# Optimization experiments

Hardware: AMD Instinct MI355X
Metric: run time of the kernel (lower is better)

## Reference

```python
import jax, jax.numpy as jnp
import numpy as np

HID = 128
SCALE = np.sqrt(HID)


def _ln(x, g, b, eps=1e-5):
    m = jnp.mean(x, axis=-1, keepdims=True)
    v = jnp.mean((x - m) ** 2, axis=-1, keepdims=True)
    return (x - m) * jax.lax.rsqrt(v + eps) * g + b


def _attention(img, txt, Wi, bi, Wt, bt, g1, b1, Wq, bq, Wk, bk, Wv, bv, g2, b2, Wo, bo):
    # img: [..., S, image_dim], txt: [..., S, text_dim] -> [..., S, HID]
    c = img @ Wi.T + bi + txt @ Wt.T + bt
    c = _ln(c, g1, b1)
    q = c @ Wq.T + bq
    k = c @ Wk.T + bk
    v = c @ Wv.T + bv
    s = jnp.einsum('...qd,...kd->...qk', q, k) / (SCALE + 1e-8)
    a = jax.nn.softmax(s, axis=-1)
    a = a + 1e-10
    a = a / jnp.sum(a, axis=-1, keepdims=True)
    a = jnp.clip(a, 1e-7, 1.0)
    ctx = jnp.einsum('...qk,...kd->...qd', a, v)
    ctx = _ln(ctx, g2, b2)
    return ctx @ Wo.T + bo


def setup_inputs() -> dict:
    key = jax.random.key(0)
    ks = jax.random.split(key, 24)
    T, Q, DI, DT = 256, 64, 2048, 768

    def xavier(k, shape):
        fan_in, fan_out = shape[1], shape[0]
        lim = np.sqrt(6.0 / (fan_in + fan_out))
        return jax.random.uniform(k, shape, jnp.float32, -lim, lim)

    return {
        'support_images': jax.random.normal(ks[0], (T, 4, DI), jnp.float32),
        'support_texts': jax.random.normal(ks[1], (T, 4, DT), jnp.float32),
        'support_labels': jax.random.randint(ks[2], (T, 4), 0, 4, jnp.int64),
        'query_images': jax.random.normal(ks[3], (T, Q, DI), jnp.float32),
        'query_texts': jax.random.normal(ks[4], (T, Q, DT), jnp.float32),
        'Wi': xavier(ks[5], (HID, DI)), 'bi': jnp.zeros((HID,)),
        'Wt': xavier(ks[6], (HID, DT)), 'bt': jnp.zeros((HID,)),
        'g1': jnp.ones((HID,)), 'b1': jnp.zeros((HID,)),
        'Wq': xavier(ks[7], (HID, HID)), 'bq': jnp.zeros((HID,)),
        'Wk': xavier(ks[8], (HID, HID)), 'bk': jnp.zeros((HID,)),
        'Wv': xavier(ks[9], (HID, HID)), 'bv': jnp.zeros((HID,)),
        'g2': jnp.ones((HID,)), 'b2': jnp.zeros((HID,)),
        'Wo': xavier(ks[10], (HID, HID)), 'bo': jnp.zeros((HID,)),
    }


def reference(support_images, support_texts, support_labels, query_images, query_texts,
              Wi, bi, Wt, bt, g1, b1, Wq, bq, Wk, bk, Wv, bv, g2, b2, Wo, bo):
    p = (Wi, bi, Wt, bt, g1, b1, Wq, bq, Wk, bk, Wv, bv, g2, b2, Wo, bo)
    # Support: attention across the 4 support items of each task -> [T, 4, HID]
    support_feats = _attention(support_images, support_texts, *p)
    # Queries: source processes each query alone (seq len 1) -> add singleton seq axis
    qf = _attention(query_images[:, :, None, :], query_texts[:, :, None, :], *p)
    qf = qf[:, :, 0, :]  # [T, Q, HID]
    # Cosine-similarity prototype scoring (eps=1e-8 as in F.cosine_similarity)
    qn = qf / jnp.clip(jnp.linalg.norm(qf, axis=-1, keepdims=True), 1e-8, None)
    pn = support_feats / jnp.clip(jnp.linalg.norm(support_feats, axis=-1, keepdims=True), 1e-8, None)
    logits = jnp.einsum('tqd,tcd->tqc', qn, pn) * 10.0  # [T, Q, 4]
    return logits
```

## Files before the change

### kernel.cpp

```cpp
#include <hip/hip_runtime.h>

typedef __bf16 bf16_t;
typedef __attribute__((ext_vector_type(4))) __bf16 bf16x4;
typedef __attribute__((ext_vector_type(8))) __bf16 bf16x8;
typedef __attribute__((ext_vector_type(4))) float floatx4;

#define LN_EPS 1e-5f

__device__ __forceinline__ void dma16(const void* g, void* l) {
    __builtin_amdgcn_global_load_lds(
        (const __attribute__((address_space(1))) void*)g,
        (__attribute__((address_space(3))) void*)l, 16, 0, 0);
}

__global__ __launch_bounds__(256) void k0_prep(
    const float* __restrict__ bi, const float* __restrict__ bt,
    const float* __restrict__ Wq, const float* __restrict__ Wk,
    const float* __restrict__ Wv, const float* __restrict__ Wo,
    float* __restrict__ c_all, bf16_t* __restrict__ wbf)
{
    const int b = blockIdx.x;
    if (b < 2176) {
        int i = b * 256 + threadIdx.x;
        int c4 = i & 31;
        float4 a = ((const float4*)bi)[c4];
        float4 bb = ((const float4*)bt)[c4];
        float4 v; v.x = a.x + bb.x; v.y = a.y + bb.y; v.z = a.z + bb.z; v.w = a.w + bb.w;
        ((float4*)c_all)[i] = v;
    } else {
        int i4 = (b - 2176) * 256 + threadIdx.x;
        int which = i4 >> 12;
        int off4  = i4 & 4095;
        const float* W = (which == 0) ? Wq : (which == 1) ? Wk : (which == 2) ? Wv : Wo;
        float4 v = ((const float4*)W)[off4];
        bf16x4 pk; pk.x = (bf16_t)v.x; pk.y = (bf16_t)v.y;
                   pk.z = (bf16_t)v.z; pk.w = (bf16_t)v.w;
        *(bf16x4*)&wbf[which * 16384 + off4 * 4] = pk;
    }
}

__global__ __launch_bounds__(256, 4) void k1_gemm(
    const float* __restrict__ qimg, const float* __restrict__ qtxt,
    const float* __restrict__ simg, const float* __restrict__ stxt,
    const float* __restrict__ Wi,   const float* __restrict__ Wt,
    float* __restrict__ c_all)
{
    __shared__ float lA[64 * 32];
    __shared__ float lB[128 * 32];

    const int tid  = threadIdx.x;
    const int m0   = blockIdx.x * 64;
    const int chnk = blockIdx.y;
    const bool isq = (m0 < 16384);
    const int rb   = isq ? m0 : (m0 - 16384);
    const float* Aimg = isq ? qimg : simg;
    const float* Atxt = isq ? qtxt : stxt;

    const int wid  = tid >> 6;
    const int lane = tid & 63;
    const int quad = lane >> 4;
    const int l16  = lane & 15;
    const int wr   = wid >> 1;
    const int wc   = wid & 1;

    const int jr = lane >> 3;
    const int cA = (lane & 7) ^ jr;

    floatx4 acc[2][4];
#pragma unroll
    for (int i = 0; i < 2; ++i)
#pragma unroll
        for (int j = 0; j < 4; ++j) acc[i][j] = (floatx4)0.f;

    for (int s = 0; s < 22; ++s) {
        const int k0 = chnk * 704 + s * 32;
        const float* abase; const float* bbase; size_t lda, ldb;
        if (k0 < 2048) {
            abase = Aimg + (size_t)rb * 2048 + k0; lda = 2048;
            bbase = Wi + k0;                        ldb = 2048;
        } else {
            abase = Atxt + (size_t)rb * 768 + (k0 - 2048); lda = 768;
            bbase = Wt + (k0 - 2048);                       ldb = 768;
        }
        __syncthreads();
#pragma unroll
        for (int ii = 0; ii < 2; ++ii) {
            int i = 2 * wid + ii;
            dma16(abase + (size_t)(8 * i + jr) * lda + (cA << 2),
                  (char*)lA + i * 1024);
        }
#pragma unroll
        for (int ii = 0; ii < 4; ++ii) {
            int i = 4 * wid + ii;
            dma16(bbase + (size_t)(8 * i + jr) * ldb + (cA << 2),
                  (char*)lB + i * 1024);
        }
        __syncthreads();

        const int x7 = l16 & 7;
        bf16x8 af[2], bfr[4];
#pragma unroll
        for (int mt = 0; mt < 2; ++mt) {
            int R = wr * 32 + mt * 16 + l16;
            float4 f0 = *(const float4*)&lA[R * 32 + (((2 * quad)     ^ x7) << 2)];
            float4 f1 = *(const float4*)&lA[R * 32 + (((2 * quad + 1) ^ x7) << 2)];
            bf16x8 a;
            a[0] = (bf16_t)f0.x; a[1] = (bf16_t)f0.y; a[2] = (bf16_t)f0.z; a[3] = (bf16_t)f0.w;
            a[4] = (bf16_t)f1.x; a[5] = (bf16_t)f1.y; a[6] = (bf16_t)f1.z; a[7] = (bf16_t)f1.w;
            af[mt] = a;
        }
#pragma unroll
        for (int nt = 0; nt < 4; ++nt) {
            int R = wc * 64 + nt * 16 + l16;
            float4 f0 = *(const float4*)&lB[R * 32 + (((2 * quad)     ^ x7) << 2)];
            float4 f1 = *(const float4*)&lB[R * 32 + (((2 * quad + 1) ^ x7) << 2)];
            bf16x8 b;
            b[0] = (bf16_t)f0.x; b[1] = (bf16_t)f0.y; b[2] = (bf16_t)f0.z; b[3] = (bf16_t)f0.w;
            b[4] = (bf16_t)f1.x; b[5] = (bf16_t)f1.y; b[6] = (bf16_t)f1.z; b[7] = (bf16_t)f1.w;
            bfr[nt] = b;
        }
#pragma unroll
        for (int mt = 0; mt < 2; ++mt)
#pragma unroll
            for (int nt = 0; nt < 4; ++nt)
                acc[mt][nt] = __builtin_amdgcn_mfma_f32_16x16x32_bf16(
                    af[mt], bfr[nt], acc[mt][nt], 0, 0, 0);
    }
#pragma unroll
    for (int nt = 0; nt < 4; ++nt) {
        int col = wc * 64 + nt * 16 + l16;
#pragma unroll
        for (int mt = 0; mt < 2; ++mt)
#pragma unroll
            for (int r = 0; r < 4; ++r) {
                int row = wr * 32 + mt * 16 + quad * 4 + r;
                unsafeAtomicAdd(&c_all[(size_t)(m0 + row) * 128 + col], acc[mt][nt][r]);
            }
    }
}

#define K2_ST 136

__global__ __launch_bounds__(256) void k2_query(
    const float* __restrict__ c_all, const bf16_t* __restrict__ wbf,
    const float* __restrict__ bv, const float* __restrict__ bo,
    const float* __restrict__ g1, const float* __restrict__ b1,
    const float* __restrict__ g2, const float* __restrict__ b2,
    const float* __restrict__ pn, float* __restrict__ out)
{
    __shared__ bf16_t tT[64 * K2_ST];
    __shared__ bf16_t tW[128 * 128];
    __shared__ float  pl[4][132];

    const int tid  = threadIdx.x;
    const int wid  = tid >> 6;
    const int lane = tid & 63;
    const int quad = lane >> 4;
    const int l16  = lane & 15;
    const int task = blockIdx.x;
    const int t0   = task * 64;
    const int r0   = wid * 16;

    const bf16_t* Wvb = wbf + 2 * 16384;
    const bf16_t* Wob = wbf + 3 * 16384;

    const int jr4 = lane >> 4;
    const int jp  = lane & 15;
#pragma unroll
    for (int ii = 0; ii < 8; ++ii) {
        int i = 8 * wid + ii;
        int row = 4 * i + jr4;
        int c = jp ^ (row & 15);
        dma16(Wvb + row * 128 + c * 8, (char*)tW + i * 1024);
    }
    if (tid < 128) {
        int r = tid >> 5, c4 = tid & 31;
        *(float4*)&pl[r][c4 * 4] = *(const float4*)(pn + ((size_t)task * 4 + r) * 128 + c4 * 4);
    }

    float bvr[8], g2r[8], b2r[8], bor[8];
#pragma unroll
    for (int nt = 0; nt < 8; ++nt) {
        int col = nt * 16 + l16;
        bvr[nt] = bv[col]; g2r[nt] = g2[col]; b2r[nt] = b2[col]; bor[nt] = bo[col];
    }

    const int g8 = lane >> 3;
    const int s8 = lane & 7;
    float g1a[16], b1a[16];
#pragma unroll
    for (int mm = 0; mm < 4; ++mm) {
        *(float4*)&g1a[mm * 4] = ((const float4*)(g1 + s8 * 16))[mm];
        *(float4*)&b1a[mm * 4] = ((const float4*)(b1 + s8 * 16))[mm];
    }
#pragma unroll
    for (int p = 0; p < 2; ++p) {
        int rloc = r0 + p * 8 + g8;
        const float* src = c_all + (size_t)(t0 + rloc) * 128 + s8 * 16;
        float v[16];
#pragma unroll
        for (int mm = 0; mm < 4; ++mm) *(float4*)&v[mm * 4] = ((const float4*)src)[mm];
        float s = 0.f, q = 0.f;
#pragma unroll
        for (int m = 0; m < 16; ++m) { s += v[m]; q += v[m] * v[m]; }
#pragma unroll
        for (int m = 1; m < 8; m <<= 1) { s += __shfl_xor(s, m); q += __shfl_xor(q, m); }
        float mean = s * (1.f / 128.f);
        float var  = q * (1.f / 128.f) - mean * mean;
        float rs   = rsqrtf(var + LN_EPS);
        bf16x8 o0, o1;
#pragma unroll
        for (int m = 0; m < 8; ++m)  o0[m] = (bf16_t)((v[m] - mean) * rs * g1a[m] + b1a[m]);
#pragma unroll
        for (int m = 0; m < 8; ++m)  o1[m] = (bf16_t)((v[8 + m] - mean) * rs * g1a[8 + m] + b1a[8 + m]);
        *(bf16x8*)&tT[rloc * K2_ST + s8 * 16]     = o0;
        *(bf16x8*)&tT[rloc * K2_ST + s8 * 16 + 8] = o1;
    }
    __syncthreads();

    floatx4 acc[8];
#pragma unroll
    for (int nt = 0; nt < 8; ++nt) acc[nt] = (floatx4)0.f;
#pragma unroll
    for (int ks = 0; ks < 4; ++ks) {
        bf16x8 a = *(const bf16x8*)&tT[(r0 + l16) * K2_ST + ks * 32 + quad * 8];
#pragma unroll
        for (int nt = 0; nt < 8; ++nt) {
            bf16x8 b = *(const bf16x8*)&tW[(nt * 16 + l16) * 128 + (((ks * 4 + quad) ^ l16) << 3)];
            acc[nt] = __builtin_amdgcn_mfma_f32_16x16x32_bf16(a, b, acc[nt], 0, 0, 0);
        }
    }
#pragma unroll
    for (int nt = 0; nt < 8; ++nt)
#pragma unroll
        for (int r = 0; r < 4; ++r) acc[nt][r] += bvr[nt];

#pragma unroll
    for (int r = 0; r < 4; ++r) {
        float s = 0.f, q = 0.f;
#pragma unroll
        for (int nt = 0; nt < 8; ++nt) { float x = acc[nt][r]; s += x; q += x * x; }
#pragma unroll
        for (int m = 1; m < 16; m <<= 1) { s += __shfl_xor(s, m); q += __shfl_xor(q, m); }
        float mean = s * (1.f / 128.f);
        float var  = q * (1.f / 128.f) - mean * mean;
        float rs   = rsqrtf(var + LN_EPS);
        int row = r0 + quad * 4 + r;
#pragma unroll
        for (int nt = 0; nt < 8; ++nt)
            tT[row * K2_ST + nt * 16 + l16] = (bf16_t)((acc[nt][r] - mean) * rs * g2r[nt] + b2r[nt]);
    }
    __syncthreads();
#pragma unroll
    for (int ii = 0; ii < 8; ++ii) {
        int i = 8 * wid + ii;
        int row = 4 * i + jr4;
        int c = jp ^ (row & 15);
        dma16(Wob + row * 128 + c * 8, (char*)tW + i * 1024);
    }
    __syncthreads();

#pragma unroll
    for (int nt = 0; nt < 8; ++nt) acc[nt] = (floatx4)0.f;
#pragma unroll
    for (int ks = 0; ks < 4; ++ks) {
        bf16x8 a = *(const bf16x8*)&tT[(r0 + l16) * K2_ST + ks * 32 + quad * 8];
#pragma unroll
        for (int nt = 0; nt < 8; ++nt) {
            bf16x8 b = *(const bf16x8*)&tW[(nt * 16 + l16) * 128 + (((ks * 4 + quad) ^ l16) << 3)];
            acc[nt] = __builtin_amdgcn_mfma_f32_16x16x32_bf16(a, b, acc[nt], 0, 0, 0);
        }
    }

#pragma unroll
    for (int r = 0; r < 4; ++r) {
        float st[8]; float q = 0.f;
#pragma unroll
        for (int nt = 0; nt < 8; ++nt) {
            float x = acc[nt][r] + bor[nt]; st[nt] = x; q += x * x;
        }
#pragma unroll
        for (int m = 1; m < 16; m <<= 1) q += __shfl_xor(q, m);
        float inv = 1.f / fmaxf(sqrtf(q), 1e-8f);
        float d0 = 0.f, d1 = 0.f, d2 = 0.f, d3 = 0.f;
#pragma unroll
        for (int nt = 0; nt < 8; ++nt) {
            float xn = st[nt] * inv;
            int col = nt * 16 + l16;
            d0 += xn * pl[0][col]; d1 += xn * pl[1][col];
            d2 += xn * pl[2][col]; d3 += xn * pl[3][col];
        }
#pragma unroll
        for (int m = 1; m < 16; m <<= 1) {
            d0 += __shfl_xor(d0, m); d1 += __shfl_xor(d1, m);
            d2 += __shfl_xor(d2, m); d3 += __shfl_xor(d3, m);
        }
        if (l16 == 0) {
            int qi = r0 + quad * 4 + r;
            float* o = out + (size_t)task * 256 + qi * 4;
            o[0] = d0 * 10.f; o[1] = d1 * 10.f; o[2] = d2 * 10.f; o[3] = d3 * 10.f;
        }
    }
}

__global__ __launch_bounds__(256) void k3_support(
    const float* __restrict__ c_all, const bf16_t* __restrict__ wbf,
    const float* __restrict__ bq, const float* __restrict__ bk,
    const float* __restrict__ bv, const float* __restrict__ bo,
    const float* __restrict__ g1, const float* __restrict__ b1,
    const float* __restrict__ g2, const float* __restrict__ b2,
    float* __restrict__ pn)
{
    __shared__ float  cs[4][128];
    __shared__ bf16_t tW[128 * 128];
    __shared__ float  qkv[3][4][128];
    __shared__ float  att[4][4];
    __shared__ float  ctx[4][128];

    const int tid  = threadIdx.x;
    const int wid  = tid >> 6;
    const int lane = tid & 63;
    const int task = blockIdx.x;
    const int jr4  = lane >> 4;
    const int jp   = lane & 15;

    {
        const float* src = c_all + (size_t)(16384 + task * 4 + wid) * 128;
        float x0 = src[lane], x1 = src[64 + lane];
        float s = x0 + x1, q = x0 * x0 + x1 * x1;
#pragma unroll
        for (int m = 1; m < 64; m <<= 1) { s += __shfl_xor(s, m); q += __shfl_xor(q, m); }
        float mean = s * (1.f / 128.f);
        float var  = q * (1.f / 128.f) - mean * mean;
        float rs   = rsqrtf(var + LN_EPS);
        cs[wid][lane]      = (x0 - mean) * rs * g1[lane] + b1[lane];
        cs[wid][64 + lane] = (x1 - mean) * rs * g1[64 + lane] + b1[64 + lane];
    }

    const float* Bs[3] = { bq, bk, bv };
    for (int w = 0; w < 3; ++w) {
        __syncthreads();
#pragma unroll
        for (int ii = 0; ii < 8; ++ii) {
            int i = 8 * wid + ii;
            int row = 4 * i + jr4;
            int c = jp ^ (row & 15);
            dma16(wbf + w * 16384 + row * 128 + c * 8, (char*)tW + i * 1024);
        }
        __syncthreads();
#pragma unroll
        for (int j = 0; j < 2; ++j) {
            int o = tid + j * 256;
            int s = o >> 7, n = o & 127;
            const float4* c4 = (const float4*)cs[s];
            float acc = 0.f;
#pragma unroll
            for (int c = 0; c < 16; ++c) {
                bf16x8 wv = *(const bf16x8*)&tW[n * 128 + ((c ^ (n & 15)) << 3)];
                float4 a0 = c4[c * 2], a1 = c4[c * 2 + 1];
                acc += a0.x * (float)wv[0] + a0.y * (float)wv[1]
                     + a0.z * (float)wv[2] + a0.w * (float)wv[3]
                     + a1.x * (float)wv[4] + a1.y * (float)wv[5]
                     + a1.z * (float)wv[6] + a1.w * (float)wv[7];
            }
            qkv[w][s][n] = acc + Bs[w][n];
        }
    }
    __syncthreads();
    if (tid < 16) {
        int i = tid >> 2, j = tid & 3;
        const float4* qv = (const float4*)qkv[0][i];
        const float4* kv = (const float4*)qkv[1][j];
        float acc = 0.f;
#pragma unroll
        for (int k = 0; k < 32; ++k) {
            float4 a = qv[k], b = kv[k];
            acc += a.x * b.x + a.y * b.y + a.z * b.z + a.w * b.w;
        }
        att[i][j] = acc * (float)(1.0 / (11.313708498984761 + 1e-8));
    }
    __syncthreads();
    if (tid < 4) {
        float s0 = att[tid][0], s1 = att[tid][1], s2 = att[tid][2], s3 = att[tid][3];
        float m = fmaxf(fmaxf(s0, s1), fmaxf(s2, s3));
        float e0 = expf(s0 - m), e1 = expf(s1 - m), e2 = expf(s2 - m), e3 = expf(s3 - m);
        float se = e0 + e1 + e2 + e3;
        float a0 = e0 / se + 1e-10f, a1 = e1 / se + 1e-10f;
        float a2 = e2 / se + 1e-10f, a3 = e3 / se + 1e-10f;
        float t = a0 + a1 + a2 + a3;
        att[tid][0] = fminf(fmaxf(a0 / t, 1e-7f), 1.f);
        att[tid][1] = fminf(fmaxf(a1 / t, 1e-7f), 1.f);
        att[tid][2] = fminf(fmaxf(a2 / t, 1e-7f), 1.f);
        att[tid][3] = fminf(fmaxf(a3 / t, 1e-7f), 1.f);
    }
    __syncthreads();
#pragma unroll
    for (int j = 0; j < 2; ++j) {
        int o = tid + j * 256;
        int s = o >> 7, n = o & 127;
        ctx[s][n] = att[s][0] * qkv[2][0][n] + att[s][1] * qkv[2][1][n]
                  + att[s][2] * qkv[2][2][n] + att[s][3] * qkv[2][3][n];
    }
    __syncthreads();
    {
        float x0 = ctx[wid][lane], x1 = ctx[wid][64 + lane];
        float s = x0 + x1, q = x0 * x0 + x1 * x1;
#pragma unroll
        for (int m = 1; m < 64; m <<= 1) { s += __shfl_xor(s, m); q += __shfl_xor(q, m); }
        float mean = s * (1.f / 128.f);
        float var  = q * (1.f / 128.f) - mean * mean;
        float rs   = rsqrtf(var + LN_EPS);
        cs[wid][lane]      = (x0 - mean) * rs * g2[lane] + b2[lane];
        cs[wid][64 + lane] = (x1 - mean) * rs * g2[64 + lane] + b2[64 + lane];
    }
    __syncthreads();
#pragma unroll
    for (int ii = 0; ii < 8; ++ii) {
        int i = 8 * wid + ii;
        int row = 4 * i + jr4;
        int c = jp ^ (row & 15);
        dma16(wbf + 3 * 16384 + row * 128 + c * 8, (char*)tW + i * 1024);
    }
    __syncthreads();
#pragma unroll
    for (int j = 0; j < 2; ++j) {
        int o = tid + j * 256;
        int s = o >> 7, n = o & 127;
        const float4* c4 = (const float4*)cs[s];
        float acc = 0.f;
#pragma unroll
        for (int c = 0; c < 16; ++c) {
            bf16x8 wv = *(const bf16x8*)&tW[n * 128 + ((c ^ (n & 15)) << 3)];
            float4 a0 = c4[c * 2], a1 = c4[c * 2 + 1];
            acc += a0.x * (float)wv[0] + a0.y * (float)wv[1]
                 + a0.z * (float)wv[2] + a0.w * (float)wv[3]
                 + a1.x * (float)wv[4] + a1.y * (float)wv[5]
                 + a1.z * (float)wv[6] + a1.w * (float)wv[7];
        }
        ctx[s][n] = acc + bo[n];
    }
    __syncthreads();
    {
        float x0 = ctx[wid][lane], x1 = ctx[wid][64 + lane];
        float q = x0 * x0 + x1 * x1;
#pragma unroll
        for (int m = 1; m < 64; m <<= 1) q += __shfl_xor(q, m);
        float inv = 1.f / fmaxf(sqrtf(q), 1e-8f);
        float* dst = pn + (size_t)(task * 4 + wid) * 128;
        dst[lane]      = x0 * inv;
        dst[64 + lane] = x1 * inv;
    }
}

extern "C" void kernel_launch(void* const* d_in, const int* in_sizes, int n_in,
                              void* d_out, int out_size, void* d_ws, size_t ws_size,
                              hipStream_t stream)
{
    const float* simg = (const float*)d_in[0];
    const float* stxt = (const float*)d_in[1];
    const float* qimg = (const float*)d_in[3];
    const float* qtxt = (const float*)d_in[4];
    const float* Wi = (const float*)d_in[5];
    const float* bi = (const float*)d_in[6];
    const float* Wt = (const float*)d_in[7];
    const float* bt = (const float*)d_in[8];
    const float* g1 = (const float*)d_in[9];
    const float* b1 = (const float*)d_in[10];
    const float* Wq = (const float*)d_in[11];
    const float* bq = (const float*)d_in[12];
    const float* Wk = (const float*)d_in[13];
    const float* bk = (const float*)d_in[14];
    const float* Wv = (const float*)d_in[15];
    const float* bv = (const float*)d_in[16];
    const float* g2 = (const float*)d_in[17];
    const float* b2 = (const float*)d_in[18];
    const float* Wo = (const float*)d_in[19];
    const float* bo = (const float*)d_in[20];
    float* out = (float*)d_out;

    float*  c_all = (float*)d_ws;
    float*  pn    = c_all + (size_t)17408 * 128;
    bf16_t* wbf   = (bf16_t*)(pn + (size_t)1024 * 128);

    k0_prep<<<2240, 256, 0, stream>>>(bi, bt, Wq, Wk, Wv, Wo, c_all, wbf);
    k1_gemm<<<dim3(272, 4), 256, 0, stream>>>(qimg, qtxt, simg, stxt, Wi, Wt, c_all);
    k3_support<<<256, 256, 0, stream>>>(c_all, wbf, bq, bk, bv, bo, g1, b1, g2, b2, pn);
    k2_query<<<256, 256, 0, stream>>>(c_all, wbf, bv, bo, g1, b1, g2, b2, pn, out);
}
```

Measured before the change: 325.6 us.

## Pre-convert Wi/Wt to bf16, load GEMM operands directly, fuse support and query kernels

The prep kernel now also converts Wi and Wt to bf16. The big projection GEMM drops its LDS staging and barriers and loads fp32 activations and bf16 weights straight from global memory into MFMA fragments. This halves weight traffic and removes the per-step syncthreads, but each wave now issues uncoalesced 32-byte row-strided loads with no reuse through shared memory. The support-attention and query kernels are merged into one launch that keeps the prototypes in LDS, which removes a launch and the pn round-trip through global memory.

```diff
diff --git a/kernel.cpp b/kernel.cpp
--- a/kernel.cpp
+++ b/kernel.cpp
@@ -13,10 +13,14 @@
         (__attribute__((address_space(3))) void*)l, 16, 0, 0);
 }
 
+#define WBF_WI 65536
+#define WBF_WT (65536 + 262144)
+
 __global__ __launch_bounds__(256) void k0_prep(
     const float* __restrict__ bi, const float* __restrict__ bt,
     const float* __restrict__ Wq, const float* __restrict__ Wk,
     const float* __restrict__ Wv, const float* __restrict__ Wo,
+    const float* __restrict__ Wi, const float* __restrict__ Wt,
     float* __restrict__ c_all, bf16_t* __restrict__ wbf)
 {
     const int b = blockIdx.x;
@@ -29,24 +33,64 @@
         ((float4*)c_all)[i] = v;
     } else {
         int i4 = (b - 2176) * 256 + threadIdx.x;
-        int which = i4 >> 12;
-        int off4  = i4 & 4095;
-        const float* W = (which == 0) ? Wq : (which == 1) ? Wk : (which == 2) ? Wv : Wo;
-        float4 v = ((const float4*)W)[off4];
+        const float* src; int dst;
+        if (i4 < 16384) {
+            int which = i4 >> 12, off4 = i4 & 4095;
+            src = ((which == 0) ? Wq : (which == 1) ? Wk : (which == 2) ? Wv : Wo) + off4 * 4;
+            dst = which * 16384 + off4 * 4;
+        } else if (i4 < 16384 + 65536) {
+            int off4 = i4 - 16384;
+            src = Wi + off4 * 4; dst = WBF_WI + off4 * 4;
+        } else {
+            int off4 = i4 - (16384 + 65536);
+            src = Wt + off4 * 4; dst = WBF_WT + off4 * 4;
+        }
+        float4 v = *(const float4*)src;
         bf16x4 pk; pk.x = (bf16_t)v.x; pk.y = (bf16_t)v.y;
                    pk.z = (bf16_t)v.z; pk.w = (bf16_t)v.w;
-        *(bf16x4*)&wbf[which * 16384 + off4 * 4] = pk;
+        *(bf16x4*)&wbf[dst] = pk;
     }
 }
+
+#define K1_MFMA8(FA0, FA1)                                                     \
+    acc[0][0] = __builtin_amdgcn_mfma_f32_16x16x32_bf16(FA0, fb0, acc[0][0], 0, 0, 0); \
+    acc[0][1] = __builtin_amdgcn_mfma_f32_16x16x32_bf16(FA0, fb1, acc[0][1], 0, 0, 0); \
+    acc[0][2] = __builtin_amdgcn_mfma_f32_16x16x32_bf16(FA0, fb2, acc[0][2], 0, 0, 0); \
+    acc[0][3] = __builtin_amdgcn_mfma_f32_16x16x32_bf16(FA0, fb3, acc[0][3], 0, 0, 0); \
+    acc[1][0] = __builtin_amdgcn_mfma_f32_16x16x32_bf16(FA1, fb0, acc[1][0], 0, 0, 0); \
+    acc[1][1] = __builtin_amdgcn_mfma_f32_16x16x32_bf16(FA1, fb1, acc[1][1], 0, 0, 0); \
+    acc[1][2] = __builtin_amdgcn_mfma_f32_16x16x32_bf16(FA1, fb2, acc[1][2], 0, 0, 0); \
+    acc[1][3] = __builtin_amdgcn_mfma_f32_16x16x32_bf16(FA1, fb3, acc[1][3], 0, 0, 0);
+
+#define K1_BODY(A0, A1, B0, B1, B2, B3, K)                                     \
+    {                                                                          \
+        float4 p00 = *(const float4*)((A0) + (K));                             \
+        float4 p01 = *(const float4*)((A0) + (K) + 4);                         \
+        float4 p10 = *(const float4*)((A1) + (K));                             \
+        float4 p11 = *(const float4*)((A1) + (K) + 4);                         \
+        bf16x8 fb0 = *(const bf16x8*)((B0) + (K));                             \
+        bf16x8 fb1 = *(const bf16x8*)((B1) + (K));                             \
+        bf16x8 fb2 = *(const bf16x8*)((B2) + (K));                             \
+        bf16x8 fb3 = *(const bf16x8*)((B3) + (K));                             \
+        bf16x8 fa0, fa1;                                                       \
+        fa0[0] = (bf16_t)p00.x; fa0[1] = (bf16_t)p00.y;                        \
+        fa0[2] = (bf16_t)p00.z; fa0[3] = (bf16_t)p00.w;                        \
+        fa0[4] = (bf16_t)p01.x; fa0[5] = (bf16_t)p01.y;                        \
+        fa0[6] = (bf16_t)p01.z; fa0[7] = (bf16_t)p01.w;                        \
+        fa1[0] = (bf16_t)p10.x; fa1[1] = (bf16_t)p10.y;                        \
+        fa1[2] = (bf16_t)p10.z; fa1[3] = (bf16_t)p10.w;                        \
+        fa1[4] = (bf16_t)p11.x; fa1[5] = (bf16_t)p11.y;                        \
+        fa1[6] = (bf16_t)p11.z; fa1[7] = (bf16_t)p11.w;                        \
+        K1_MFMA8(fa0, fa1)                                                     \
+    }
 
 __global__ __launch_bounds__(256, 4) void k1_gemm(
     const float* __restrict__ qimg, const float* __restrict__ qtxt,
     const float* __restrict__ simg, const float* __restrict__ stxt,
-    const float* __restrict__ Wi,   const float* __restrict__ Wt,
-    float* __restrict__ c_all)
+    const bf16_t* __restrict__ wbf, float* __restrict__ c_all)
 {
-    __shared__ float lA[64 * 32];
-    __shared__ float lB[128 * 32];
+    const bf16_t* Wib = wbf + WBF_WI;
+    const bf16_t* Wtb = wbf + WBF_WT;
 
     const int tid  = threadIdx.x;
     const int m0   = blockIdx.x * 64;
@@ -63,8 +107,8 @@
     const int wr   = wid >> 1;
     const int wc   = wid & 1;
 
-    const int jr = lane >> 3;
-    const int cA = (lane & 7) ^ jr;
+    const int ar0 = rb + wr * 32 + l16;
+    const int bc0 = wc * 64 + l16;
 
     floatx4 acc[2][4];
 #pragma unroll
@@ -72,60 +116,35 @@
 #pragma unroll
         for (int j = 0; j < 4; ++j) acc[i][j] = (floatx4)0.f;
 
-    for (int s = 0; s < 22; ++s) {
-        const int k0 = chnk * 704 + s * 32;
-        const float* abase; const float* bbase; size_t lda, ldb;
-        if (k0 < 2048) {
-            abase = Aimg + (size_t)rb * 2048 + k0; lda = 2048;
-            bbase = Wi + k0;                        ldb = 2048;
-        } else {
-            abase = Atxt + (size_t)rb * 768 + (k0 - 2048); lda = 768;
-            bbase = Wt + (k0 - 2048);                       ldb = 768;
-        }
-        __syncthreads();
-#pragma unroll
-        for (int ii = 0; ii < 2; ++ii) {
-            int i = 2 * wid + ii;
-            dma16(abase + (size_t)(8 * i + jr) * lda + (cA << 2),
-                  (char*)lA + i * 1024);
-        }
-#pragma unroll
-        for (int ii = 0; ii < 4; ++ii) {
-            int i = 4 * wid + ii;
-            dma16(bbase + (size_t)(8 * i + jr) * ldb + (cA << 2),
-                  (char*)lB + i * 1024);
-        }
-        __syncthreads();
-
-        const int x7 = l16 & 7;
-        bf16x8 af[2], bfr[4];
-#pragma unroll
-        for (int mt = 0; mt < 2; ++mt) {
-            int R = wr * 32 + mt * 16 + l16;
-            float4 f0 = *(const float4*)&lA[R * 32 + (((2 * quad)     ^ x7) << 2)];
-            float4 f1 = *(const float4*)&lA[R * 32 + (((2 * quad + 1) ^ x7) << 2)];
-            bf16x8 a;
-            a[0] = (bf16_t)f0.x; a[1] = (bf16_t)f0.y; a[2] = (bf16_t)f0.z; a[3] = (bf16_t)f0.w;
-            a[4] = (bf16_t)f1.x; a[5] = (bf16_t)f1.y; a[6] = (bf16_t)f1.z; a[7] = (bf16_t)f1.w;
-            af[mt] = a;
-        }
-#pragma unroll
-        for (int nt = 0; nt < 4; ++nt) {
-            int R = wc * 64 + nt * 16 + l16;
-            float4 f0 = *(const float4*)&lB[R * 32 + (((2 * quad)     ^ x7) << 2)];
-            float4 f1 = *(const float4*)&lB[R * 32 + (((2 * quad + 1) ^ x7) << 2)];
-            bf16x8 b;
-            b[0] = (bf16_t)f0.x; b[1] = (bf16_t)f0.y; b[2] = (bf16_t)f0.z; b[3] = (bf16_t)f0.w;
-            b[4] = (bf16_t)f1.x; b[5] = (bf16_t)f1.y; b[6] = (bf16_t)f1.z; b[7] = (bf16_t)f1.w;
-            bfr[nt] = b;
-        }
-#pragma unroll
-        for (int mt = 0; mt < 2; ++mt)
-#pragma unroll
-            for (int nt = 0; nt < 4; ++nt)
-                acc[mt][nt] = __builtin_amdgcn_mfma_f32_16x16x32_bf16(
-                    af[mt], bfr[nt], acc[mt][nt], 0, 0, 0);
-    }
+    const int kb = chnk * 704;
+    const int ke = kb + 704;
+
+    const int ie = (ke < 2048) ? ke : 2048;
+    if (kb < ie) {
+        const float*  a0 = Aimg + (size_t)ar0 * 2048 + quad * 8 + kb;
+        const float*  a1 = a0 + (size_t)16 * 2048;
+        const bf16_t* b0 = Wib + (size_t)bc0 * 2048 + quad * 8 + kb;
+        const bf16_t* b1 = b0 + (size_t)16 * 2048;
+        const bf16_t* b2 = b0 + (size_t)32 * 2048;
+        const bf16_t* b3 = b0 + (size_t)48 * 2048;
+        const int n = ie - kb;
+#pragma unroll 2
+        for (int k = 0; k < n; k += 32) K1_BODY(a0, a1, b0, b1, b2, b3, k)
+    }
+    const int ts = (kb > 2048) ? kb : 2048;
+    if (ts < ke) {
+        const int off = ts - 2048;
+        const float*  a0 = Atxt + (size_t)ar0 * 768 + quad * 8 + off;
+        const float*  a1 = a0 + (size_t)16 * 768;
+        const bf16_t* b0 = Wtb + (size_t)bc0 * 768 + quad * 8 + off;
+        const bf16_t* b1 = b0 + (size_t)16 * 768;
+        const bf16_t* b2 = b0 + (size_t)32 * 768;
+        const bf16_t* b3 = b0 + (size_t)48 * 768;
+        const int n = ke - ts;
+#pragma unroll 2
+        for (int k = 0; k < n; k += 32) K1_BODY(a0, a1, b0, b1, b2, b3, k)
+    }
+
 #pragma unroll
     for (int nt = 0; nt < 4; ++nt) {
         int col = wc * 64 + nt * 16 + l16;
@@ -141,15 +160,19 @@
 
 #define K2_ST 136
 
-__global__ __launch_bounds__(256) void k2_query(
+__global__ __launch_bounds__(256) void k2_fused(
     const float* __restrict__ c_all, const bf16_t* __restrict__ wbf,
+    const float* __restrict__ bq, const float* __restrict__ bk,
     const float* __restrict__ bv, const float* __restrict__ bo,
     const float* __restrict__ g1, const float* __restrict__ b1,
     const float* __restrict__ g2, const float* __restrict__ b2,
-    const float* __restrict__ pn, float* __restrict__ out)
+    float* __restrict__ out)
 {
     __shared__ bf16_t tT[64 * K2_ST];
     __shared__ bf16_t tW[128 * 128];
+    __shared__ float  cs[4][128];
+    __shared__ float  qkv[3][4][128];
+    __shared__ float  att[4][4];
     __shared__ float  pl[4][132];
 
     const int tid  = threadIdx.x;
@@ -160,22 +183,15 @@
     const int task = blockIdx.x;
     const int t0   = task * 64;
     const int r0   = wid * 16;
-
-    const bf16_t* Wvb = wbf + 2 * 16384;
-    const bf16_t* Wob = wbf + 3 * 16384;
-
-    const int jr4 = lane >> 4;
-    const int jp  = lane & 15;
+    const int jr4  = lane >> 4;
+    const int jp   = lane & 15;
+
 #pragma unroll
     for (int ii = 0; ii < 8; ++ii) {
         int i = 8 * wid + ii;
         int row = 4 * i + jr4;
         int c = jp ^ (row & 15);
-        dma16(Wvb + row * 128 + c * 8, (char*)tW + i * 1024);
-    }
-    if (tid < 128) {
-        int r = tid >> 5, c4 = tid & 31;
-        *(float4*)&pl[r][c4 * 4] = *(const float4*)(pn + ((size_t)task * 4 + r) * 128 + c4 * 4);
+        dma16(wbf + 0 * 16384 + row * 128 + c * 8, (char*)tW + i * 1024);
     }
 
     float bvr[8], g2r[8], b2r[8], bor[8];
@@ -185,145 +201,38 @@
         bvr[nt] = bv[col]; g2r[nt] = g2[col]; b2r[nt] = b2[col]; bor[nt] = bo[col];
     }
 
-    const int g8 = lane >> 3;
-    const int s8 = lane & 7;
-    float g1a[16], b1a[16];
-#pragma unroll
-    for (int mm = 0; mm < 4; ++mm) {
-        *(float4*)&g1a[mm * 4] = ((const float4*)(g1 + s8 * 16))[mm];
-        *(float4*)&b1a[mm * 4] = ((const float4*)(b1 + s8 * 16))[mm];
-    }
-#pragma unroll
-    for (int p = 0; p < 2; ++p) {
-        int rloc = r0 + p * 8 + g8;
-        const float* src = c_all + (size_t)(t0 + rloc) * 128 + s8 * 16;
-        float v[16];
-#pragma unroll
-        for (int mm = 0; mm < 4; ++mm) *(float4*)&v[mm * 4] = ((const float4*)src)[mm];
-        float s = 0.f, q = 0.f;
-#pragma unroll
-        for (int m = 0; m < 16; ++m) { s += v[m]; q += v[m] * v[m]; }
-#pragma unroll
-        for (int m = 1; m < 8; m <<= 1) { s += __shfl_xor(s, m); q += __shfl_xor(q, m); }
-        float mean = s * (1.f / 128.f);
-        float var  = q * (1.f / 128.f) - mean * mean;
-        float rs   = rsqrtf(var + LN_EPS);
-        bf16x8 o0, o1;
-#pragma unroll
-        for (int m = 0; m < 8; ++m)  o0[m] = (bf16_t)((v[m] - mean) * rs * g1a[m] + b1a[m]);
-#pragma unroll
-        for (int m = 0; m < 8; ++m)  o1[m] = (bf16_t)((v[8 + m] - mean) * rs * g1a[8 + m] + b1a[8 + m]);
-        *(bf16x8*)&tT[rloc * K2_ST + s8 * 16]     = o0;
-        *(bf16x8*)&tT[rloc * K2_ST + s8 * 16 + 8] = o1;
-    }
-    __syncthreads();
-
-    floatx4 acc[8];
-#pragma unroll
-    for (int nt = 0; nt < 8; ++nt) acc[nt] = (floatx4)0.f;
-#pragma unroll
-    for (int ks = 0; ks < 4; ++ks) {
-        bf16x8 a = *(const bf16x8*)&tT[(r0 + l16) * K2_ST + ks * 32 + quad * 8];
-#pragma unroll
-        for (int nt = 0; nt < 8; ++nt) {
-            bf16x8 b = *(const bf16x8*)&tW[(nt * 16 + l16) * 128 + (((ks * 4 + quad) ^ l16) << 3)];
-            acc[nt] = __builtin_amdgcn_mfma_f32_16x16x32_bf16(a, b, acc[nt], 0, 0, 0);
-        }
-    }
-#pragma unroll
-    for (int nt = 0; nt < 8; ++nt)
-#pragma unroll
-        for (int r = 0; r < 4; ++r) acc[nt][r] += bvr[nt];
-
-#pragma unroll
-    for (int r = 0; r < 4; ++r) {
-        float s = 0.f, q = 0.f;
-#pragma unroll
-        for (int nt = 0; nt < 8; ++nt) { float x = acc[nt][r]; s += x; q += x * x; }
-#pragma unroll
-        for (int m = 1; m < 16; m <<= 1) { s += __shfl_xor(s, m); q += __shfl_xor(q, m); }
-        float mean = s * (1.f / 128.f);
-        float var  = q * (1.f / 128.f) - mean * mean;
-        float rs   = rsqrtf(var + LN_EPS);
-        int row = r0 + quad * 4 + r;
-#pragma unroll
-        for (int nt = 0; nt < 8; ++nt)
-            tT[row * K2_ST + nt * 16 + l16] = (bf16_t)((acc[nt][r] - mean) * rs * g2r[nt] + b2r[nt]);
-    }
-    __syncthreads();
-#pragma unroll
-    for (int ii = 0; ii < 8; ++ii) {
-        int i = 8 * wid + ii;
-        int row = 4 * i + jr4;
-        int c = jp ^ (row & 15);
-        dma16(Wob + row * 128 + c * 8, (char*)tW + i * 1024);
-    }
-    __syncthreads();
-
-#pragma unroll
-    for (int nt = 0; nt < 8; ++nt) acc[nt] = (floatx4)0.f;
-#pragma unroll
-    for (int ks = 0; ks < 4; ++ks) {
-        bf16x8 a = *(const bf16x8*)&tT[(r0 + l16) * K2_ST + ks * 32 + quad * 8];
-#pragma unroll
-        for (int nt = 0; nt < 8; ++nt) {
-            bf16x8 b = *(const bf16x8*)&tW[(nt * 16 + l16) * 128 + (((ks * 4 + quad) ^ l16) << 3)];
-            acc[nt] = __builtin_amdgcn_mfma_f32_16x16x32_bf16(a, b, acc[nt], 0, 0, 0);
-        }
-    }
-
-#pragma unroll
-    for (int r = 0; r < 4; ++r) {
-        float st[8]; float q = 0.f;
-#pragma unroll
-        for (int nt = 0; nt < 8; ++nt) {
-            float x = acc[nt][r] + bor[nt]; st[nt] = x; q += x * x;
-        }
-#pragma unroll
-        for (int m = 1; m < 16; m <<= 1) q += __shfl_xor(q, m);
-        float inv = 1.f / fmaxf(sqrtf(q), 1e-8f);
-        float d0 = 0.f, d1 = 0.f, d2 = 0.f, d3 = 0.f;
-#pragma unroll
-        for (int nt = 0; nt < 8; ++nt) {
-            float xn = st[nt] * inv;
-            int col = nt * 16 + l16;
-            d0 += xn * pl[0][col]; d1 += xn * pl[1][col];
-            d2 += xn * pl[2][col]; d3 += xn * pl[3][col];
-        }
-#pragma unroll
-        for (int m = 1; m < 16; m <<= 1) {
-            d0 += __shfl_xor(d0, m); d1 += __shfl_xor(d1, m);
-            d2 += __shfl_xor(d2, m); d3 += __shfl_xor(d3, m);
-        }
-        if (l16 == 0) {
-            int qi = r0 + quad * 4 + r;
-            float* o = out + (size_t)task * 256 + qi * 4;
-            o[0] = d0 * 10.f; o[1] = d1 * 10.f; o[2] = d2 * 10.f; o[3] = d3 * 10.f;
-        }
-    }
-}
-
-__global__ __launch_bounds__(256) void k3_support(
-    const float* __restrict__ c_all, const bf16_t* __restrict__ wbf,
-    const float* __restrict__ bq, const float* __restrict__ bk,
-    const float* __restrict__ bv, const float* __restrict__ bo,
-    const float* __restrict__ g1, const float* __restrict__ b1,
-    const float* __restrict__ g2, const float* __restrict__ b2,
-    float* __restrict__ pn)
-{
-    __shared__ float  cs[4][128];
-    __shared__ bf16_t tW[128 * 128];
-    __shared__ float  qkv[3][4][128];
-    __shared__ float  att[4][4];
-    __shared__ float  ctx[4][128];
-
-    const int tid  = threadIdx.x;
-    const int wid  = tid >> 6;
-    const int lane = tid & 63;
-    const int task = blockIdx.x;
-    const int jr4  = lane >> 4;
-    const int jp   = lane & 15;
-
+    {
+        const int g8 = lane >> 3, s8 = lane & 7;
+        float g1a[16], b1a[16];
+#pragma unroll
+        for (int mm = 0; mm < 4; ++mm) {
+            *(float4*)&g1a[mm * 4] = ((const float4*)(g1 + s8 * 16))[mm];
+            *(float4*)&b1a[mm * 4] = ((const float4*)(b1 + s8 * 16))[mm];
+        }
+#pragma unroll
+        for (int p = 0; p < 2; ++p) {
+            int rloc = r0 + p * 8 + g8;
+            const float* src = c_all + (size_t)(t0 + rloc) * 128 + s8 * 16;
+            float v[16];
+#pragma unroll
+            for (int mm = 0; mm < 4; ++mm) *(float4*)&v[mm * 4] = ((const float4*)src)[mm];
+            float s = 0.f, q = 0.f;
+#pragma unroll
+            for (int m = 0; m < 16; ++m) { s += v[m]; q += v[m] * v[m]; }
+#pragma unroll
+            for (int m = 1; m < 8; m <<= 1) { s += __shfl_xor(s, m); q += __shfl_xor(q, m); }
+            float mean = s * (1.f / 128.f);
+            float var  = q * (1.f / 128.f) - mean * mean;
+            float rs   = rsqrtf(var + LN_EPS);
+            bf16x8 o0, o1;
+#pragma unroll
+            for (int m = 0; m < 8; ++m) o0[m] = (bf16_t)((v[m] - mean) * rs * g1a[m] + b1a[m]);
+#pragma unroll
+            for (int m = 0; m < 8; ++m) o1[m] = (bf16_t)((v[8 + m] - mean) * rs * g1a[8 + m] + b1a[8 + m]);
+            *(bf16x8*)&tT[rloc * K2_ST + s8 * 16]     = o0;
+            *(bf16x8*)&tT[rloc * K2_ST + s8 * 16 + 8] = o1;
+        }
+    }
     {
         const float* src = c_all + (size_t)(16384 + task * 4 + wid) * 128;
         float x0 = src[lane], x1 = src[64 + lane];
@@ -336,50 +245,127 @@
         cs[wid][lane]      = (x0 - mean) * rs * g1[lane] + b1[lane];
         cs[wid][64 + lane] = (x1 - mean) * rs * g1[64 + lane] + b1[64 + lane];
     }
-
-    const float* Bs[3] = { bq, bk, bv };
-    for (int w = 0; w < 3; ++w) {
-        __syncthreads();
-#pragma unroll
-        for (int ii = 0; ii < 8; ++ii) {
-            int i = 8 * wid + ii;
-            int row = 4 * i + jr4;
-            int c = jp ^ (row & 15);
-            dma16(wbf + w * 16384 + row * 128 + c * 8, (char*)tW + i * 1024);
-        }
-        __syncthreads();
-#pragma unroll
-        for (int j = 0; j < 2; ++j) {
-            int o = tid + j * 256;
-            int s = o >> 7, n = o & 127;
-            const float4* c4 = (const float4*)cs[s];
-            float acc = 0.f;
-#pragma unroll
-            for (int c = 0; c < 16; ++c) {
-                bf16x8 wv = *(const bf16x8*)&tW[n * 128 + ((c ^ (n & 15)) << 3)];
-                float4 a0 = c4[c * 2], a1 = c4[c * 2 + 1];
-                acc += a0.x * (float)wv[0] + a0.y * (float)wv[1]
-                     + a0.z * (float)wv[2] + a0.w * (float)wv[3]
-                     + a1.x * (float)wv[4] + a1.y * (float)wv[5]
-                     + a1.z * (float)wv[6] + a1.w * (float)wv[7];
-            }
-            qkv[w][s][n] = acc + Bs[w][n];
-        }
-    }
-    __syncthreads();
+    __syncthreads();
+
+#pragma unroll
+    for (int j = 0; j < 2; ++j) {
+        int o = tid + j * 256, s = o >> 7, n = o & 127;
+        const float4* c4 = (const float4*)cs[s];
+        float acc = 0.f;
+#pragma unroll
+        for (int c = 0; c < 16; ++c) {
+            bf16x8 wv = *(const bf16x8*)&tW[n * 128 + ((c ^ (n & 15)) << 3)];
+            float4 a0 = c4[c * 2], a1 = c4[c * 2 + 1];
+            acc += a0.x * (float)wv[0] + a0.y * (float)wv[1]
+                 + a0.z * (float)wv[2] + a0.w * (float)wv[3]
+                 + a1.x * (float)wv[4] + a1.y * (float)wv[5]
+                 + a1.z * (float)wv[6] + a1.w * (float)wv[7];
+        }
+        qkv[0][s][n] = acc + bq[n];
+    }
+    __syncthreads();
+#pragma unroll
+    for (int ii = 0; ii < 8; ++ii) {
+        int i = 8 * wid + ii;
+        int row = 4 * i + jr4;
+        int c = jp ^ (row & 15);
+        dma16(wbf + 1 * 16384 + row * 128 + c * 8, (char*)tW + i * 1024);
+    }
+    __syncthreads();
+#pragma unroll
+    for (int j = 0; j < 2; ++j) {
+        int o = tid + j * 256, s = o >> 7, n = o & 127;
+        const float4* c4 = (const float4*)cs[s];
+        float acc = 0.f;
+#pragma unroll
+        for (int c = 0; c < 16; ++c) {
+            bf16x8 wv = *(const bf16x8*)&tW[n * 128 + ((c ^ (n & 15)) << 3)];
+            float4 a0 = c4[c * 2], a1 = c4[c * 2 + 1];
+            acc += a0.x * (float)wv[0] + a0.y * (float)wv[1]
+                 + a0.z * (float)wv[2] + a0.w * (float)wv[3]
+                 + a1.x * (float)wv[4] + a1.y * (float)wv[5]
+                 + a1.z * (float)wv[6] + a1.w * (float)wv[7];
+        }
+        qkv[1][s][n] = acc + bk[n];
+    }
+    __syncthreads();
+#pragma unroll
+    for (int ii = 0; ii < 8; ++ii) {
+        int i = 8 * wid + ii;
+        int row = 4 * i + jr4;
+        int c = jp ^ (row & 15);
+        dma16(wbf + 2 * 16384 + row * 128 + c * 8, (char*)tW + i * 1024);
+    }
+    __syncthreads();
+
+    floatx4 acc[8];
+#pragma unroll
+    for (int nt = 0; nt < 8; ++nt) acc[nt] = (floatx4)0.f;
+#pragma unroll
+    for (int ks = 0; ks < 4; ++ks) {
+        bf16x8 a = *(const bf16x8*)&tT[(r0 + l16) * K2_ST + ks * 32 + quad * 8];
+#pragma unroll
+        for (int nt = 0; nt < 8; ++nt) {
+            bf16x8 b = *(const bf16x8*)&tW[(nt * 16 + l16) * 128 + (((ks * 4 + quad) ^ l16) << 3)];
+            acc[nt] = __builtin_amdgcn_mfma_f32_16x16x32_bf16(a, b, acc[nt], 0, 0, 0);
+        }
+    }
+#pragma unroll
+    for (int nt = 0; nt < 8; ++nt)
+#pragma unroll
+        for (int r = 0; r < 4; ++r) acc[nt][r] += bvr[nt];
+
+#pragma unroll
+    for (int j = 0; j < 2; ++j) {
+        int o = tid + j * 256, s = o >> 7, n = o & 127;
+        const float4* c4 = (const float4*)cs[s];
+        float a = 0.f;
+#pragma unroll
+        for (int c = 0; c < 16; ++c) {
+            bf16x8 wv = *(const bf16x8*)&tW[n * 128 + ((c ^ (n & 15)) << 3)];
+            float4 a0 = c4[c * 2], a1 = c4[c * 2 + 1];
+            a += a0.x * (float)wv[0] + a0.y * (float)wv[1]
+               + a0.z * (float)wv[2] + a0.w * (float)wv[3]
+               + a1.x * (float)wv[4] + a1.y * (float)wv[5]
+               + a1.z * (float)wv[6] + a1.w * (float)wv[7];
+        }
+        qkv[2][s][n] = a + bv[n];
+    }
     if (tid < 16) {
         int i = tid >> 2, j = tid & 3;
         const float4* qv = (const float4*)qkv[0][i];
         const float4* kv = (const float4*)qkv[1][j];
-        float acc = 0.f;
+        float a = 0.f;
 #pragma unroll
         for (int k = 0; k < 32; ++k) {
-            float4 a = qv[k], b = kv[k];
-            acc += a.x * b.x + a.y * b.y + a.z * b.z + a.w * b.w;
-        }
-        att[i][j] = acc * (float)(1.0 / (11.313708498984761 + 1e-8));
-    }
-    __syncthreads();
+            float4 x = qv[k], y = kv[k];
+            a += x.x * y.x + x.y * y.y + x.z * y.z + x.w * y.w;
+        }
+        att[i][j] = a * (float)(1.0 / (11.313708498984761 + 1e-8));
+    }
+#pragma unroll
+    for (int r = 0; r < 4; ++r) {
+        float s = 0.f, q = 0.f;
+#pragma unroll
+        for (int nt = 0; nt < 8; ++nt) { float x = acc[nt][r]; s += x; q += x * x; }
+#pragma unroll
+        for (int m = 1; m < 16; m <<= 1) { s += __shfl_xor(s, m); q += __shfl_xor(q, m); }
+        float mean = s * (1.f / 128.f);
+        float var  = q * (1.f / 128.f) - mean * mean;
+        float rs   = rsqrtf(var + LN_EPS);
+        int row = r0 + quad * 4 + r;
+#pragma unroll
+        for (int nt = 0; nt < 8; ++nt)
+            tT[row * K2_ST + nt * 16 + l16] = (bf16_t)((acc[nt][r] - mean) * rs * g2r[nt] + b2r[nt]);
+    }
+    __syncthreads();
+#pragma unroll
+    for (int ii = 0; ii < 8; ++ii) {
+        int i = 8 * wid + ii;
+        int row = 4 * i + jr4;
+        int c = jp ^ (row & 15);
+        dma16(wbf + 3 * 16384 + row * 128 + c * 8, (char*)tW + i * 1024);
+    }
     if (tid < 4) {
         float s0 = att[tid][0], s1 = att[tid][1], s2 = att[tid][2], s3 = att[tid][3];
         float m = fmaxf(fmaxf(s0, s1), fmaxf(s2, s3));
@@ -394,16 +380,16 @@
         att[tid][3] = fminf(fmaxf(a3 / t, 1e-7f), 1.f);
     }
     __syncthreads();
+
 #pragma unroll
     for (int j = 0; j < 2; ++j) {
-        int o = tid + j * 256;
-        int s = o >> 7, n = o & 127;
-        ctx[s][n] = att[s][0] * qkv[2][0][n] + att[s][1] * qkv[2][1][n]
-                  + att[s][2] * qkv[2][2][n] + att[s][3] * qkv[2][3][n];
+        int o = tid + j * 256, s = o >> 7, n = o & 127;
+        qkv[0][s][n] = att[s][0] * qkv[2][0][n] + att[s][1] * qkv[2][1][n]
+                     + att[s][2] * qkv[2][2][n] + att[s][3] * qkv[2][3][n];
     }
     __syncthreads();
     {
-        float x0 = ctx[wid][lane], x1 = ctx[wid][64 + lane];
+        float x0 = qkv[0][wid][lane], x1 = qkv[0][wid][64 + lane];
         float s = x0 + x1, q = x0 * x0 + x1 * x1;
 #pragma unroll
         for (int m = 1; m < 64; m <<= 1) { s += __shfl_xor(s, m); q += __shfl_xor(q, m); }
@@ -414,41 +400,76 @@
         cs[wid][64 + lane] = (x1 - mean) * rs * g2[64 + lane] + b2[64 + lane];
     }
     __syncthreads();
-#pragma unroll
-    for (int ii = 0; ii < 8; ++ii) {
-        int i = 8 * wid + ii;
-        int row = 4 * i + jr4;
-        int c = jp ^ (row & 15);
-        dma16(wbf + 3 * 16384 + row * 128 + c * 8, (char*)tW + i * 1024);
-    }
-    __syncthreads();
+
 #pragma unroll
     for (int j = 0; j < 2; ++j) {
-        int o = tid + j * 256;
-        int s = o >> 7, n = o & 127;
+        int o = tid + j * 256, s = o >> 7, n = o & 127;
         const float4* c4 = (const float4*)cs[s];
-        float acc = 0.f;
+        float a = 0.f;
 #pragma unroll
         for (int c = 0; c < 16; ++c) {
             bf16x8 wv = *(const bf16x8*)&tW[n * 128 + ((c ^ (n & 15)) << 3)];
             float4 a0 = c4[c * 2], a1 = c4[c * 2 + 1];
-            acc += a0.x * (float)wv[0] + a0.y * (float)wv[1]
-                 + a0.z * (float)wv[2] + a0.w * (float)wv[3]
-                 + a1.x * (float)wv[4] + a1.y * (float)wv[5]
-                 + a1.z * (float)wv[6] + a1.w * (float)wv[7];
-        }
-        ctx[s][n] = acc + bo[n];
+            a += a0.x * (float)wv[0] + a0.y * (float)wv[1]
+               + a0.z * (float)wv[2] + a0.w * (float)wv[3]
+               + a1.x * (float)wv[4] + a1.y * (float)wv[5]
+               + a1.z * (float)wv[6] + a1.w * (float)wv[7];
+        }
+        qkv[1][s][n] = a + bo[n];
+    }
+
+    floatx4 acc2[8];
+#pragma unroll
+    for (int nt = 0; nt < 8; ++nt) acc2[nt] = (floatx4)0.f;
+#pragma unroll
+    for (int ks = 0; ks < 4; ++ks) {
+        bf16x8 a = *(const bf16x8*)&tT[(r0 + l16) * K2_ST + ks * 32 + quad * 8];
+#pragma unroll
+        for (int nt = 0; nt < 8; ++nt) {
+            bf16x8 b = *(const bf16x8*)&tW[(nt * 16 + l16) * 128 + (((ks * 4 + quad) ^ l16) << 3)];
+            acc2[nt] = __builtin_amdgcn_mfma_f32_16x16x32_bf16(a, b, acc2[nt], 0, 0, 0);
+        }
     }
     __syncthreads();
     {
-        float x0 = ctx[wid][lane], x1 = ctx[wid][64 + lane];
+        float x0 = qkv[1][wid][lane], x1 = qkv[1][wid][64 + lane];
         float q = x0 * x0 + x1 * x1;
 #pragma unroll
         for (int m = 1; m < 64; m <<= 1) q += __shfl_xor(q, m);
         float inv = 1.f / fmaxf(sqrtf(q), 1e-8f);
-        float* dst = pn + (size_t)(task * 4 + wid) * 128;
-        dst[lane]      = x0 * inv;
-        dst[64 + lane] = x1 * inv;
+        pl[wid][lane]      = x0 * inv;
+        pl[wid][64 + lane] = x1 * inv;
+    }
+    __syncthreads();
+
+#pragma unroll
+    for (int r = 0; r < 4; ++r) {
+        float st[8]; float q = 0.f;
+#pragma unroll
+        for (int nt = 0; nt < 8; ++nt) {
+            float x = acc2[nt][r] + bor[nt]; st[nt] = x; q += x * x;
+        }
+#pragma unroll
+        for (int m = 1; m < 16; m <<= 1) q += __shfl_xor(q, m);
+        float inv = 1.f / fmaxf(sqrtf(q), 1e-8f);
+        float d0 = 0.f, d1 = 0.f, d2 = 0.f, d3 = 0.f;
+#pragma unroll
+        for (int nt = 0; nt < 8; ++nt) {
+            float xn = st[nt] * inv;
+            int col = nt * 16 + l16;
+            d0 += xn * pl[0][col]; d1 += xn * pl[1][col];
+            d2 += xn * pl[2][col]; d3 += xn * pl[3][col];
+        }
+#pragma unroll
+        for (int m = 1; m < 16; m <<= 1) {
+            d0 += __shfl_xor(d0, m); d1 += __shfl_xor(d1, m);
+            d2 += __shfl_xor(d2, m); d3 += __shfl_xor(d3, m);
+        }
+        if (l16 == 0) {
+            int qi = r0 + quad * 4 + r;
+            float* o = out + (size_t)task * 256 + qi * 4;
+            o[0] = d0 * 10.f; o[1] = d1 * 10.f; o[2] = d2 * 10.f; o[3] = d3 * 10.f;
+        }
     }
 }
 
@@ -479,11 +500,9 @@
     float* out = (float*)d_out;
 
     float*  c_all = (float*)d_ws;
-    float*  pn    = c_all + (size_t)17408 * 128;
-    bf16_t* wbf   = (bf16_t*)(pn + (size_t)1024 * 128);
-
-    k0_prep<<<2240, 256, 0, stream>>>(bi, bt, Wq, Wk, Wv, Wo, c_all, wbf);
-    k1_gemm<<<dim3(272, 4), 256, 0, stream>>>(qimg, qtxt, simg, stxt, Wi, Wt, c_all);
-    k3_support<<<256, 256, 0, stream>>>(c_all, wbf, bq, bk, bv, bo, g1, b1, g2, b2, pn);
-    k2_query<<<256, 256, 0, stream>>>(c_all, wbf, bv, bo, g1, b1, g2, b2, pn, out);
+    bf16_t* wbf   = (bf16_t*)(c_all + (size_t)17408 * 128);
+
+    k0_prep<<<2592, 256, 0, stream>>>(bi, bt, Wq, Wk, Wv, Wo, Wi, Wt, c_all, wbf);
+    k1_gemm<<<dim3(272, 4), 256, 0, stream>>>(qimg, qtxt, simg, stxt, wbf, c_all);
+    k2_fused<<<256, 256, 0, stream>>>(c_all, wbf, bq, bk, bv, bo, g1, b1, g2, b2, out);
 }
```

Result: slower. 360.0 us (+10.6%).
